# Optimization experiments

Measured on AMD Instinct MI355X. Metric: run time of the kernel, lower is better.

The kernel has to match this reference:

```python
import jax, jax.numpy as jnp
import numpy as np

H, N, F = 10, 200000, 128
HID, C = 256, 100
NEG_SLOPE = 0.2

def _leaky(x):
    return jnp.where(x >= 0, x, NEG_SLOPE * x)

def _prelu(x, a):
    return jnp.where(x >= 0, x, a * x)

def setup_inputs() -> dict:
    key = jax.random.key(0)
    ks = jax.random.split(key, 12)
    inp = {
        "features": jax.random.normal(ks[0], (H, N, F), dtype=jnp.float32),
        "label_emb": jax.random.normal(ks[1], (N, C), dtype=jnp.float32),
        # lr_att: Linear(2F, 1) -> weight as [2F] vector + scalar bias
        "W_att": jax.random.normal(ks[2], (2 * F,), dtype=jnp.float32) * 0.05,
        "b_att": jnp.zeros((), dtype=jnp.float32),
        # lr_output = FeedForwardNetII(F, HID, C, n_layers=2): Dense(F,HID), PReLU, Dense(HID,C)
        "Wo1": jax.random.normal(ks[3], (F, HID), dtype=jnp.float32) * 0.05,
        "bo1": jnp.zeros((HID,), dtype=jnp.float32),
        "ao": jnp.asarray(0.25, dtype=jnp.float32),
        "Wo2": jax.random.normal(ks[4], (HID, C), dtype=jnp.float32) * 0.05,
        "bo2": jnp.zeros((C,), dtype=jnp.float32),
        # label_fc = FeedForwardNet(C, HID, C, n_layers=2): Linear(C,HID), PReLU, Linear(HID,C)
        "Wl1": jax.random.normal(ks[5], (C, HID), dtype=jnp.float32) * 0.05,
        "bl1": jnp.zeros((HID,), dtype=jnp.float32),
        "al": jnp.asarray(0.25, dtype=jnp.float32),
        "Wl2": jax.random.normal(ks[6], (HID, C), dtype=jnp.float32) * 0.05,
        "bl2": jnp.zeros((C,), dtype=jnp.float32),
    }
    return inp

def reference(features, label_emb, W_att, b_att, Wo1, bo1, ao, Wo2, bo2,
              Wl1, bl1, al, Wl2, bl2):
    # features: [H, N, F]; dropouts are identity (p=0, eval mode)
    nF = features.shape[-1]
    W1, W2 = W_att[:nF], W_att[nF:]  # cat([history, x_i]) @ W_att == history@W1 + x_i@W2
    x0 = features[0]
    scores = [_leaky(x0 @ (W1 + W2) + b_att)]  # hop 0: cat([x0, x0])
    for i in range(1, features.shape[0]):
        hist_att = jax.nn.softmax(jnp.stack(scores, axis=1), axis=1)  # [N, i]
        history = jnp.einsum('ni,inf->nf', hist_att, features[:i])    # [N, F]
        scores.append(_leaky(history @ W1 + features[i] @ W2 + b_att))
    att = jax.nn.softmax(jnp.stack(scores, axis=1), axis=1)           # [N, H]
    right = jnp.einsum('ni,inf->nf', att, features)                   # [N, F]
    # lr_output: Dense -> PReLU -> Dense
    out = _prelu(right @ Wo1 + bo1, ao) @ Wo2 + bo2                   # [N, C]
    # label branch: label_fc(label_emb)
    out = out + (_prelu(label_emb @ Wl1 + bl1, al) @ Wl2 + bl2)
    return out
```

## Files before the change

kernel.cpp:

```cpp
#include <hip/hip_runtime.h>
#include <hip/hip_bf16.h>
#include <cstddef>

#define NHOP 10
#define NN 200000
#define FF 128
#define HIDD 256
#define CCC 100
#define NEG_SLOPE_C 0.2f

typedef __attribute__((ext_vector_type(8))) short bf16x8;
typedef __attribute__((ext_vector_type(4))) short bf16x4;
typedef __attribute__((ext_vector_type(4))) float f32x4;

__device__ __forceinline__ short f2bfs(float x){
  return __builtin_bit_cast(short, __float2bfloat16(x));
}
__device__ __forceinline__ float bf2f(short s){
  return __uint_as_float(((unsigned)(unsigned short)s) << 16);
}
__device__ __forceinline__ f32x4 mfma16(bf16x8 a, bf16x8 b, f32x4 c){
  return __builtin_amdgcn_mfma_f32_16x16x32_bf16(a, b, c, 0, 0, 0);
}
__device__ __forceinline__ float leakyf(float x){ return x >= 0.f ? x : NEG_SLOPE_C*x; }

__global__ __launch_bounds__(256) void prep_weights(
    const float* __restrict__ Wo1, const float* __restrict__ Wl1,
    const float* __restrict__ Wo2, const float* __restrict__ Wl2,
    unsigned short* __restrict__ Wo1T, unsigned short* __restrict__ Wl1T,
    unsigned short* __restrict__ Wo2T, unsigned short* __restrict__ Wl2T)
{
  const int id = blockIdx.x*256 + threadIdx.x;
  {
    const int c = id >> 7, k = id & 127;
    Wo1T[id] = (unsigned short)f2bfs(Wo1[(size_t)k*HIDD + c]);
    Wl1T[id] = (k < CCC) ? (unsigned short)f2bfs(Wl1[(size_t)k*HIDD + c]) : 0;
  }
  if (id < 112*256){
    const int c = id >> 8, k = id & 255;
    Wo2T[id] = (c < CCC) ? (unsigned short)f2bfs(Wo2[(size_t)k*CCC + c]) : 0;
    Wl2T[id] = (c < CCC) ? (unsigned short)f2bfs(Wl2[(size_t)k*CCC + c]) : 0;
  }
}

__global__ __launch_bounds__(256) void attn_right_kernel(
    const float* __restrict__ feat,
    const float* __restrict__ Watt,
    const float* __restrict__ batt,
    unsigned short* __restrict__ rightb)
{
  const int lane = threadIdx.x & 63;
  const int w = threadIdx.x >> 6;
  const int nl = lane >> 4, fl = lane & 15;
  const int n = blockIdx.x*16 + w*4 + nl;

  const float4 w1a = *reinterpret_cast<const float4*>(Watt + fl*4);
  const float4 w1b = *reinterpret_cast<const float4*>(Watt + 64 + fl*4);
  const float4 w2a = *reinterpret_cast<const float4*>(Watt + FF + fl*4);
  const float4 w2b = *reinterpret_cast<const float4*>(Watt + FF + 64 + fl*4);
  const float b = batt[0];

  float p1[NHOP], p2[NHOP];
  bf16x8 fbf[NHOP];
  const float* fp = feat + (size_t)n*FF;
  #pragma unroll
  for (int i=0;i<NHOP;i++){
    const float* hp = fp + (size_t)i*((size_t)NN*FF);
    const float4 va = *reinterpret_cast<const float4*>(hp + fl*4);
    const float4 vb = *reinterpret_cast<const float4*>(hp + 64 + fl*4);
    p1[i] = va.x*w1a.x + va.y*w1a.y + va.z*w1a.z + va.w*w1a.w
          + vb.x*w1b.x + vb.y*w1b.y + vb.z*w1b.z + vb.w*w1b.w;
    p2[i] = va.x*w2a.x + va.y*w2a.y + va.z*w2a.z + va.w*w2a.w
          + vb.x*w2b.x + vb.y*w2b.y + vb.z*w2b.z + vb.w*w2b.w;
    fbf[i][0]=f2bfs(va.x); fbf[i][1]=f2bfs(va.y); fbf[i][2]=f2bfs(va.z); fbf[i][3]=f2bfs(va.w);
    fbf[i][4]=f2bfs(vb.x); fbf[i][5]=f2bfs(vb.y); fbf[i][6]=f2bfs(vb.z); fbf[i][7]=f2bfs(vb.w);
  }
  #pragma unroll
  for (int m=8;m>0;m>>=1){
    #pragma unroll
    for (int i=0;i<NHOP;i++){
      p1[i] += __shfl_xor(p1[i], m, 64);
      p2[i] += __shfl_xor(p2[i], m, 64);
    }
  }
  float sc[NHOP];
  sc[0] = leakyf(p1[0] + p2[0] + b);
  #pragma unroll
  for (int i=1;i<NHOP;i++){
    float mx = sc[0];
    #pragma unroll
    for (int j=1;j<i;j++) mx = fmaxf(mx, sc[j]);
    float Z = 0.f, hs = 0.f;
    #pragma unroll
    for (int j=0;j<i;j++){
      const float e = __expf(sc[j]-mx);
      Z += e;
      hs = fmaf(e, p1[j], hs);
    }
    sc[i] = leakyf(hs/Z + p2[i] + b);
  }
  float mx = sc[0];
  #pragma unroll
  for (int j=1;j<NHOP;j++) mx = fmaxf(mx, sc[j]);
  float Z = 0.f;
  float e[NHOP];
  #pragma unroll
  for (int j=0;j<NHOP;j++){ e[j] = __expf(sc[j]-mx); Z += e[j]; }
  const float inv = 1.f/Z;
  float racc[8];
  #pragma unroll
  for (int u=0;u<8;u++) racc[u] = 0.f;
  #pragma unroll
  for (int j=0;j<NHOP;j++){
    const float a = e[j]*inv;
    #pragma unroll
    for (int u=0;u<8;u++) racc[u] = fmaf(a, bf2f(fbf[j][u]), racc[u]);
  }
  bf16x4 sa, sb;
  sa[0]=f2bfs(racc[0]); sa[1]=f2bfs(racc[1]); sa[2]=f2bfs(racc[2]); sa[3]=f2bfs(racc[3]);
  sb[0]=f2bfs(racc[4]); sb[1]=f2bfs(racc[5]); sb[2]=f2bfs(racc[6]); sb[3]=f2bfs(racc[7]);
  *reinterpret_cast<bf16x4*>(rightb + (size_t)n*FF + fl*4) = sa;
  *reinterpret_cast<bf16x4*>(rightb + (size_t)n*FF + 64 + fl*4) = sb;
}

__device__ __forceinline__ void mlp_branch(
    const unsigned short* sA, unsigned short* sH,
    const unsigned short* __restrict__ W1T, const float* __restrict__ b1, const float alpha,
    const unsigned short* __restrict__ W2T,
    f32x4 (&o)[2][4], const int w, const int lr, const int lq)
{
  bf16x8 B[4][4];
  float b1c[4];
  #pragma unroll
  for (int ctl=0; ctl<4; ++ctl){
    const int c = (4*w+ctl)*16 + lr;
    b1c[ctl] = b1[c];
    #pragma unroll
    for (int kk=0; kk<4; ++kk)
      B[ctl][kk] = *reinterpret_cast<const bf16x8*>(W1T + (size_t)c*128 + kk*32 + lq*8);
  }
  #pragma unroll
  for (int nt=0; nt<4; ++nt){
    f32x4 h[4];
    #pragma unroll
    for (int ctl=0; ctl<4; ++ctl) h[ctl] = (f32x4){0.f,0.f,0.f,0.f};
    const int row = nt*16 + lr;
    #pragma unroll
    for (int kk=0; kk<4; ++kk){
      const bf16x8 a = *reinterpret_cast<const bf16x8*>(
          (const char*)sA + row*256 + ((kk*64 + lq*16) ^ ((row&7)<<4)));
      #pragma unroll
      for (int ctl=0; ctl<4; ++ctl)
        h[ctl] = mfma16(a, B[ctl][kk], h[ctl]);
    }
    #pragma unroll
    for (int ctl=0; ctl<4; ++ctl){
      const int c = (4*w+ctl)*16 + lr;
      #pragma unroll
      for (int j=0; j<4; ++j){
        float v = h[ctl][j] + b1c[ctl];
        v = v >= 0.f ? v : alpha*v;
        const int n = nt*16 + lq*4 + j;
        *reinterpret_cast<unsigned short*>(
            (char*)sH + n*512 + ((2*c) ^ ((n&7)<<4))) = (unsigned short)f2bfs(v);
      }
    }
  }
  __syncthreads();
  #pragma unroll
  for (int i2=0; i2<2; ++i2){
    const int ct2 = 2*w + i2;
    if (ct2 < 7){
      bf16x8 b2[8];
      #pragma unroll
      for (int kk=0; kk<8; ++kk)
        b2[kk] = *reinterpret_cast<const bf16x8*>(W2T + (size_t)(ct2*16+lr)*256 + kk*32 + lq*8);
      #pragma unroll
      for (int nt=0; nt<4; ++nt){
        const int row = nt*16 + lr;
        #pragma unroll
        for (int kk=0; kk<8; ++kk){
          const bf16x8 a2 = *reinterpret_cast<const bf16x8*>(
              (const char*)sH + row*512 + ((kk*64 + lq*16) ^ ((row&7)<<4)));
          o[i2][nt] = mfma16(a2, b2[kk], o[i2][nt]);
        }
      }
    }
  }
}

__global__ __launch_bounds__(256) void mlp_mfma_kernel(
    const unsigned short* __restrict__ rightb, const float* __restrict__ label,
    const unsigned short* __restrict__ Wo1T, const float* __restrict__ bo1, const float* __restrict__ aop,
    const unsigned short* __restrict__ Wo2T, const float* __restrict__ bo2,
    const unsigned short* __restrict__ Wl1T, const float* __restrict__ bl1, const float* __restrict__ alp,
    const unsigned short* __restrict__ Wl2T, const float* __restrict__ bl2,
    float* __restrict__ out)
{
  __shared__ __align__(16) unsigned short sA[64*128];
  __shared__ __align__(16) unsigned short sH[64*256];
  const int t = threadIdx.x;
  const int w = t >> 6, lane = t & 63, lr = lane & 15, lq = lane >> 4;
  const size_t nb = (size_t)blockIdx.x * 64;

  f32x4 o[2][4];
  #pragma unroll
  for (int i2=0; i2<2; ++i2){
    const int ct2 = 2*w + i2;
    const int c2 = ct2*16 + lr;
    const float init = (ct2 < 7 && c2 < CCC) ? (bo2[c2] + bl2[c2]) : 0.f;
    #pragma unroll
    for (int nt=0; nt<4; ++nt) o[i2][nt] = (f32x4){init, init, init, init};
  }

  {
    const unsigned short* src = rightb + nb*FF;
    #pragma unroll
    for (int i=0;i<4;i++){
      const int chunk = t + 256*i;
      const int row = chunk >> 4, cs = chunk & 15;
      const bf16x8 v = *reinterpret_cast<const bf16x8*>(src + row*FF + cs*8);
      *reinterpret_cast<bf16x8*>((char*)sA + row*256 + ((cs*16) ^ ((row&7)<<4))) = v;
    }
  }
  __syncthreads();
  mlp_branch(sA, sH, Wo1T, bo1, aop[0], Wo2T, o, w, lr, lq);

  {
    #pragma unroll
    for (int i=0;i<7;i++){
      const int idx = t + 256*i;
      if (idx < 1600){
        const int row = idx/25, c0 = (idx%25)*4;
        const float4 v = *reinterpret_cast<const float4*>(label + (nb+row)*CCC + c0);
        bf16x4 p;
        p[0] = f2bfs(v.x); p[1] = f2bfs(v.y);
        p[2] = f2bfs(v.z); p[3] = f2bfs(v.w);
        *reinterpret_cast<bf16x4*>((char*)sA + row*256 + ((2*c0) ^ ((row&7)<<4))) = p;
      }
    }
    for (int idx = t; idx < 448; idx += 256){
      const int row = idx/7, ch = idx%7;
      *reinterpret_cast<bf16x4*>((char*)sA + row*256 + ((200 + 8*ch) ^ ((row&7)<<4))) = (bf16x4){0,0,0,0};
    }
  }
  __syncthreads();
  mlp_branch(sA, sH, Wl1T, bl1, alp[0], Wl2T, o, w, lr, lq);

  #pragma unroll
  for (int i2=0; i2<2; ++i2){
    const int ct2 = 2*w + i2;
    const int c2 = ct2*16 + lr;
    if (ct2 < 7 && c2 < CCC){
      #pragma unroll
      for (int nt=0; nt<4; ++nt){
        #pragma unroll
        for (int j=0; j<4; ++j){
          const int n = nt*16 + lq*4 + j;
          out[(nb + n)*CCC + c2] = o[i2][nt][j];
        }
      }
    }
  }
}

extern "C" void kernel_launch(void* const* d_in, const int* in_sizes, int n_in,
                              void* d_out, int out_size, void* d_ws, size_t ws_size,
                              hipStream_t stream) {
  const float* feat  = (const float*)d_in[0];
  const float* label = (const float*)d_in[1];
  const float* Watt  = (const float*)d_in[2];
  const float* batt  = (const float*)d_in[3];
  const float* Wo1   = (const float*)d_in[4];
  const float* bo1   = (const float*)d_in[5];
  const float* aop   = (const float*)d_in[6];
  const float* Wo2   = (const float*)d_in[7];
  const float* bo2   = (const float*)d_in[8];
  const float* Wl1   = (const float*)d_in[9];
  const float* bl1   = (const float*)d_in[10];
  const float* alp   = (const float*)d_in[11];
  const float* Wl2   = (const float*)d_in[12];
  const float* bl2   = (const float*)d_in[13];
  float* out = (float*)d_out;

  unsigned short* rightb = (unsigned short*)d_ws;
  unsigned short* Wo1T = rightb + (size_t)NN*FF;
  unsigned short* Wl1T = Wo1T + 256*128;
  unsigned short* Wo2T = Wl1T + 256*128;
  unsigned short* Wl2T = Wo2T + 112*256;

  prep_weights<<<128, 256, 0, stream>>>(Wo1, Wl1, Wo2, Wl2, Wo1T, Wl1T, Wo2T, Wl2T);
  attn_right_kernel<<<NN/16, 256, 0, stream>>>(feat, Watt, batt, rightb);
  mlp_mfma_kernel<<<NN/64, 256, 0, stream>>>(rightb, label,
                                             Wo1T, bo1, aop, Wo2T, bo2,
                                             Wl1T, bl1, alp, Wl2T, bl2, out);
}
```

Baseline: 346.6 us.

## Split second MLP GEMM across waves by node rows instead of output columns

```diff
diff --git a/kernel.cpp b/kernel.cpp
--- a/kernel.cpp
+++ b/kernel.cpp
@@ -123,11 +123,10 @@
   *reinterpret_cast<bf16x4*>(rightb + (size_t)n*FF + 64 + fl*4) = sb;
 }
 
-__device__ __forceinline__ void mlp_branch(
+__device__ __forceinline__ void gemm1_colsplit(
     const unsigned short* sA, unsigned short* sH,
     const unsigned short* __restrict__ W1T, const float* __restrict__ b1, const float alpha,
-    const unsigned short* __restrict__ W2T,
-    f32x4 (&o)[2][4], const int w, const int lr, const int lq)
+    const int w, const int lr, const int lq)
 {
   bf16x8 B[4][4];
   float b1c[4];
@@ -166,26 +165,27 @@
       }
     }
   }
-  __syncthreads();
-  #pragma unroll
-  for (int i2=0; i2<2; ++i2){
-    const int ct2 = 2*w + i2;
-    if (ct2 < 7){
-      bf16x8 b2[8];
-      #pragma unroll
-      for (int kk=0; kk<8; ++kk)
-        b2[kk] = *reinterpret_cast<const bf16x8*>(W2T + (size_t)(ct2*16+lr)*256 + kk*32 + lq*8);
-      #pragma unroll
-      for (int nt=0; nt<4; ++nt){
-        const int row = nt*16 + lr;
-        #pragma unroll
-        for (int kk=0; kk<8; ++kk){
-          const bf16x8 a2 = *reinterpret_cast<const bf16x8*>(
-              (const char*)sH + row*512 + ((kk*64 + lq*16) ^ ((row&7)<<4)));
-          o[i2][nt] = mfma16(a2, b2[kk], o[i2][nt]);
-        }
-      }
-    }
+}
+
+__device__ __forceinline__ void gemm2_nodesplit(const unsigned short* sH,
+    const unsigned short* __restrict__ W2T, f32x4 (&o)[7],
+    const int w, const int lr, const int lq)
+{
+  const int row = w*16 + lr;
+  bf16x8 a2[8];
+  #pragma unroll
+  for (int kk=0; kk<8; ++kk)
+    a2[kk] = *reinterpret_cast<const bf16x8*>(
+        (const char*)sH + row*512 + ((kk*64 + lq*16) ^ ((row&7)<<4)));
+  #pragma unroll
+  for (int ct=0; ct<7; ++ct){
+    bf16x8 b2[8];
+    #pragma unroll
+    for (int kk=0; kk<8; ++kk)
+      b2[kk] = *reinterpret_cast<const bf16x8*>(W2T + (size_t)(ct*16+lr)*256 + kk*32 + lq*8);
+    #pragma unroll
+    for (int kk=0; kk<8; ++kk)
+      o[ct] = mfma16(a2[kk], b2[kk], o[ct]);
   }
 }
 
@@ -203,14 +203,12 @@
   const int w = t >> 6, lane = t & 63, lr = lane & 15, lq = lane >> 4;
   const size_t nb = (size_t)blockIdx.x * 64;
 
-  f32x4 o[2][4];
-  #pragma unroll
-  for (int i2=0; i2<2; ++i2){
-    const int ct2 = 2*w + i2;
-    const int c2 = ct2*16 + lr;
-    const float init = (ct2 < 7 && c2 < CCC) ? (bo2[c2] + bl2[c2]) : 0.f;
-    #pragma unroll
-    for (int nt=0; nt<4; ++nt) o[i2][nt] = (f32x4){init, init, init, init};
+  f32x4 o[7];
+  #pragma unroll
+  for (int ct=0; ct<7; ++ct){
+    const int c2 = ct*16 + lr;
+    const float init = (c2 < CCC) ? (bo2[c2] + bl2[c2]) : 0.f;
+    o[ct] = (f32x4){init, init, init, init};
   }
 
   {
@@ -224,7 +222,9 @@
     }
   }
   __syncthreads();
-  mlp_branch(sA, sH, Wo1T, bo1, aop[0], Wo2T, o, w, lr, lq);
+
+  gemm1_colsplit(sA, sH, Wo1T, bo1, aop[0], w, lr, lq);
+  __syncthreads();
 
   {
     #pragma unroll
@@ -244,21 +244,21 @@
       *reinterpret_cast<bf16x4*>((char*)sA + row*256 + ((200 + 8*ch) ^ ((row&7)<<4))) = (bf16x4){0,0,0,0};
     }
   }
-  __syncthreads();
-  mlp_branch(sA, sH, Wl1T, bl1, alp[0], Wl2T, o, w, lr, lq);
-
-  #pragma unroll
-  for (int i2=0; i2<2; ++i2){
-    const int ct2 = 2*w + i2;
-    const int c2 = ct2*16 + lr;
-    if (ct2 < 7 && c2 < CCC){
+  gemm2_nodesplit(sH, Wo2T, o, w, lr, lq);
+  __syncthreads();
+
+  gemm1_colsplit(sA, sH, Wl1T, bl1, alp[0], w, lr, lq);
+  __syncthreads();
+  gemm2_nodesplit(sH, Wl2T, o, w, lr, lq);
+
+  #pragma unroll
+  for (int ct=0; ct<7; ++ct){
+    const int c2 = ct*16 + lr;
+    if (c2 < CCC){
       #pragma unroll
-      for (int nt=0; nt<4; ++nt){
-        #pragma unroll
-        for (int j=0; j<4; ++j){
-          const int n = nt*16 + lq*4 + j;
-          out[(nb + n)*CCC + c2] = o[i2][nt][j];
-        }
+      for (int j=0; j<4; ++j){
+        const int n = w*16 + lq*4 + j;
+        out[(nb + n)*CCC + c2] = o[ct][j];
       }
     }
   }
```

Result: slower. 446.1 us (+28.7%).

## Fuse attention and MLP into one kernel with 16-row tiles

Applied to the files above, without the earlier changes.

```diff
diff --git a/kernel.cpp b/kernel.cpp
--- a/kernel.cpp
+++ b/kernel.cpp
@@ -43,91 +43,10 @@
   }
 }
 
-__global__ __launch_bounds__(256) void attn_right_kernel(
-    const float* __restrict__ feat,
-    const float* __restrict__ Watt,
-    const float* __restrict__ batt,
-    unsigned short* __restrict__ rightb)
-{
-  const int lane = threadIdx.x & 63;
-  const int w = threadIdx.x >> 6;
-  const int nl = lane >> 4, fl = lane & 15;
-  const int n = blockIdx.x*16 + w*4 + nl;
-
-  const float4 w1a = *reinterpret_cast<const float4*>(Watt + fl*4);
-  const float4 w1b = *reinterpret_cast<const float4*>(Watt + 64 + fl*4);
-  const float4 w2a = *reinterpret_cast<const float4*>(Watt + FF + fl*4);
-  const float4 w2b = *reinterpret_cast<const float4*>(Watt + FF + 64 + fl*4);
-  const float b = batt[0];
-
-  float p1[NHOP], p2[NHOP];
-  bf16x8 fbf[NHOP];
-  const float* fp = feat + (size_t)n*FF;
-  #pragma unroll
-  for (int i=0;i<NHOP;i++){
-    const float* hp = fp + (size_t)i*((size_t)NN*FF);
-    const float4 va = *reinterpret_cast<const float4*>(hp + fl*4);
-    const float4 vb = *reinterpret_cast<const float4*>(hp + 64 + fl*4);
-    p1[i] = va.x*w1a.x + va.y*w1a.y + va.z*w1a.z + va.w*w1a.w
-          + vb.x*w1b.x + vb.y*w1b.y + vb.z*w1b.z + vb.w*w1b.w;
-    p2[i] = va.x*w2a.x + va.y*w2a.y + va.z*w2a.z + va.w*w2a.w
-          + vb.x*w2b.x + vb.y*w2b.y + vb.z*w2b.z + vb.w*w2b.w;
-    fbf[i][0]=f2bfs(va.x); fbf[i][1]=f2bfs(va.y); fbf[i][2]=f2bfs(va.z); fbf[i][3]=f2bfs(va.w);
-    fbf[i][4]=f2bfs(vb.x); fbf[i][5]=f2bfs(vb.y); fbf[i][6]=f2bfs(vb.z); fbf[i][7]=f2bfs(vb.w);
-  }
-  #pragma unroll
-  for (int m=8;m>0;m>>=1){
-    #pragma unroll
-    for (int i=0;i<NHOP;i++){
-      p1[i] += __shfl_xor(p1[i], m, 64);
-      p2[i] += __shfl_xor(p2[i], m, 64);
-    }
-  }
-  float sc[NHOP];
-  sc[0] = leakyf(p1[0] + p2[0] + b);
-  #pragma unroll
-  for (int i=1;i<NHOP;i++){
-    float mx = sc[0];
-    #pragma unroll
-    for (int j=1;j<i;j++) mx = fmaxf(mx, sc[j]);
-    float Z = 0.f, hs = 0.f;
-    #pragma unroll
-    for (int j=0;j<i;j++){
-      const float e = __expf(sc[j]-mx);
-      Z += e;
-      hs = fmaf(e, p1[j], hs);
-    }
-    sc[i] = leakyf(hs/Z + p2[i] + b);
-  }
-  float mx = sc[0];
-  #pragma unroll
-  for (int j=1;j<NHOP;j++) mx = fmaxf(mx, sc[j]);
-  float Z = 0.f;
-  float e[NHOP];
-  #pragma unroll
-  for (int j=0;j<NHOP;j++){ e[j] = __expf(sc[j]-mx); Z += e[j]; }
-  const float inv = 1.f/Z;
-  float racc[8];
-  #pragma unroll
-  for (int u=0;u<8;u++) racc[u] = 0.f;
-  #pragma unroll
-  for (int j=0;j<NHOP;j++){
-    const float a = e[j]*inv;
-    #pragma unroll
-    for (int u=0;u<8;u++) racc[u] = fmaf(a, bf2f(fbf[j][u]), racc[u]);
-  }
-  bf16x4 sa, sb;
-  sa[0]=f2bfs(racc[0]); sa[1]=f2bfs(racc[1]); sa[2]=f2bfs(racc[2]); sa[3]=f2bfs(racc[3]);
-  sb[0]=f2bfs(racc[4]); sb[1]=f2bfs(racc[5]); sb[2]=f2bfs(racc[6]); sb[3]=f2bfs(racc[7]);
-  *reinterpret_cast<bf16x4*>(rightb + (size_t)n*FF + fl*4) = sa;
-  *reinterpret_cast<bf16x4*>(rightb + (size_t)n*FF + 64 + fl*4) = sb;
-}
-
-__device__ __forceinline__ void mlp_branch(
+__device__ __forceinline__ void g1_16(
     const unsigned short* sA, unsigned short* sH,
     const unsigned short* __restrict__ W1T, const float* __restrict__ b1, const float alpha,
-    const unsigned short* __restrict__ W2T,
-    f32x4 (&o)[2][4], const int w, const int lr, const int lq)
+    const int w, const int lr, const int lq)
 {
   bf16x8 B[4][4];
   float b1c[4];
@@ -139,126 +58,186 @@
     for (int kk=0; kk<4; ++kk)
       B[ctl][kk] = *reinterpret_cast<const bf16x8*>(W1T + (size_t)c*128 + kk*32 + lq*8);
   }
-  #pragma unroll
-  for (int nt=0; nt<4; ++nt){
-    f32x4 h[4];
-    #pragma unroll
-    for (int ctl=0; ctl<4; ++ctl) h[ctl] = (f32x4){0.f,0.f,0.f,0.f};
-    const int row = nt*16 + lr;
-    #pragma unroll
-    for (int kk=0; kk<4; ++kk){
-      const bf16x8 a = *reinterpret_cast<const bf16x8*>(
-          (const char*)sA + row*256 + ((kk*64 + lq*16) ^ ((row&7)<<4)));
-      #pragma unroll
-      for (int ctl=0; ctl<4; ++ctl)
-        h[ctl] = mfma16(a, B[ctl][kk], h[ctl]);
-    }
-    #pragma unroll
-    for (int ctl=0; ctl<4; ++ctl){
-      const int c = (4*w+ctl)*16 + lr;
-      #pragma unroll
-      for (int j=0; j<4; ++j){
-        float v = h[ctl][j] + b1c[ctl];
-        v = v >= 0.f ? v : alpha*v;
-        const int n = nt*16 + lq*4 + j;
-        *reinterpret_cast<unsigned short*>(
-            (char*)sH + n*512 + ((2*c) ^ ((n&7)<<4))) = (unsigned short)f2bfs(v);
-      }
-    }
-  }
-  __syncthreads();
+  f32x4 h[4];
+  #pragma unroll
+  for (int ctl=0; ctl<4; ++ctl) h[ctl] = (f32x4){0.f,0.f,0.f,0.f};
+  #pragma unroll
+  for (int kk=0; kk<4; ++kk){
+    const bf16x8 a = *reinterpret_cast<const bf16x8*>(
+        (const char*)sA + lr*256 + ((kk*64 + lq*16) ^ ((lr&7)<<4)));
+    #pragma unroll
+    for (int ctl=0; ctl<4; ++ctl)
+      h[ctl] = mfma16(a, B[ctl][kk], h[ctl]);
+  }
+  #pragma unroll
+  for (int ctl=0; ctl<4; ++ctl){
+    const int c = (4*w+ctl)*16 + lr;
+    #pragma unroll
+    for (int j=0; j<4; ++j){
+      float v = h[ctl][j] + b1c[ctl];
+      v = v >= 0.f ? v : alpha*v;
+      const int n = lq*4 + j;
+      *reinterpret_cast<unsigned short*>(
+          (char*)sH + n*512 + ((2*c) ^ ((n&7)<<4))) = (unsigned short)f2bfs(v);
+    }
+  }
+}
+
+__device__ __forceinline__ void g2_16(const unsigned short* sH,
+    const unsigned short* __restrict__ W2T, f32x4 (&o)[2],
+    const int w, const int lr, const int lq)
+{
+  bf16x8 a2[8];
+  #pragma unroll
+  for (int kk=0; kk<8; ++kk)
+    a2[kk] = *reinterpret_cast<const bf16x8*>(
+        (const char*)sH + lr*512 + ((kk*64 + lq*16) ^ ((lr&7)<<4)));
   #pragma unroll
   for (int i2=0; i2<2; ++i2){
-    const int ct2 = 2*w + i2;
+    const int ct2 = w + 4*i2;
     if (ct2 < 7){
-      bf16x8 b2[8];
-      #pragma unroll
-      for (int kk=0; kk<8; ++kk)
-        b2[kk] = *reinterpret_cast<const bf16x8*>(W2T + (size_t)(ct2*16+lr)*256 + kk*32 + lq*8);
-      #pragma unroll
-      for (int nt=0; nt<4; ++nt){
-        const int row = nt*16 + lr;
-        #pragma unroll
-        for (int kk=0; kk<8; ++kk){
-          const bf16x8 a2 = *reinterpret_cast<const bf16x8*>(
-              (const char*)sH + row*512 + ((kk*64 + lq*16) ^ ((row&7)<<4)));
-          o[i2][nt] = mfma16(a2, b2[kk], o[i2][nt]);
-        }
-      }
-    }
-  }
-}
-
-__global__ __launch_bounds__(256) void mlp_mfma_kernel(
-    const unsigned short* __restrict__ rightb, const float* __restrict__ label,
+      #pragma unroll
+      for (int kk=0; kk<8; ++kk){
+        const bf16x8 b2 = *reinterpret_cast<const bf16x8*>(
+            W2T + (size_t)(ct2*16+lr)*256 + kk*32 + lq*8);
+        o[i2] = mfma16(a2[kk], b2, o[i2]);
+      }
+    }
+  }
+}
+
+__global__ __launch_bounds__(256) void gamlp_fused16(
+    const float* __restrict__ feat, const float* __restrict__ label,
+    const float* __restrict__ Watt, const float* __restrict__ batt,
     const unsigned short* __restrict__ Wo1T, const float* __restrict__ bo1, const float* __restrict__ aop,
     const unsigned short* __restrict__ Wo2T, const float* __restrict__ bo2,
     const unsigned short* __restrict__ Wl1T, const float* __restrict__ bl1, const float* __restrict__ alp,
     const unsigned short* __restrict__ Wl2T, const float* __restrict__ bl2,
     float* __restrict__ out)
 {
-  __shared__ __align__(16) unsigned short sA[64*128];
-  __shared__ __align__(16) unsigned short sH[64*256];
+  __shared__ __align__(16) unsigned short sA[16*128];
+  __shared__ __align__(16) unsigned short sH[16*256];
   const int t = threadIdx.x;
-  const int w = t >> 6, lane = t & 63, lr = lane & 15, lq = lane >> 4;
-  const size_t nb = (size_t)blockIdx.x * 64;
-
-  f32x4 o[2][4];
+  const int w = t >> 6, lane = t & 63;
+  const int nl = lane >> 4, fl = lane & 15;
+  const int lr = lane & 15, lq = lane >> 4;
+  const size_t nb = (size_t)blockIdx.x * 16;
+
+  {
+    const int n = (int)nb + w*4 + nl;
+    const float4 w1a = *reinterpret_cast<const float4*>(Watt + fl*4);
+    const float4 w1b = *reinterpret_cast<const float4*>(Watt + 64 + fl*4);
+    const float4 w2a = *reinterpret_cast<const float4*>(Watt + FF + fl*4);
+    const float4 w2b = *reinterpret_cast<const float4*>(Watt + FF + 64 + fl*4);
+    const float b = batt[0];
+
+    float p1[NHOP], p2[NHOP];
+    bf16x8 fbf[NHOP];
+    const float* fp = feat + (size_t)n*FF;
+    #pragma unroll
+    for (int i=0;i<NHOP;i++){
+      const float* hp = fp + (size_t)i*((size_t)NN*FF);
+      const float4 va = *reinterpret_cast<const float4*>(hp + fl*4);
+      const float4 vb = *reinterpret_cast<const float4*>(hp + 64 + fl*4);
+      p1[i] = va.x*w1a.x + va.y*w1a.y + va.z*w1a.z + va.w*w1a.w
+            + vb.x*w1b.x + vb.y*w1b.y + vb.z*w1b.z + vb.w*w1b.w;
+      p2[i] = va.x*w2a.x + va.y*w2a.y + va.z*w2a.z + va.w*w2a.w
+            + vb.x*w2b.x + vb.y*w2b.y + vb.z*w2b.z + vb.w*w2b.w;
+      fbf[i][0]=f2bfs(va.x); fbf[i][1]=f2bfs(va.y); fbf[i][2]=f2bfs(va.z); fbf[i][3]=f2bfs(va.w);
+      fbf[i][4]=f2bfs(vb.x); fbf[i][5]=f2bfs(vb.y); fbf[i][6]=f2bfs(vb.z); fbf[i][7]=f2bfs(vb.w);
+    }
+    #pragma unroll
+    for (int m=8;m>0;m>>=1){
+      #pragma unroll
+      for (int i=0;i<NHOP;i++){
+        p1[i] += __shfl_xor(p1[i], m, 64);
+        p2[i] += __shfl_xor(p2[i], m, 64);
+      }
+    }
+    float sc[NHOP];
+    sc[0] = leakyf(p1[0] + p2[0] + b);
+    #pragma unroll
+    for (int i=1;i<NHOP;i++){
+      float mx = sc[0];
+      #pragma unroll
+      for (int j=1;j<i;j++) mx = fmaxf(mx, sc[j]);
+      float Z = 0.f, hs = 0.f;
+      #pragma unroll
+      for (int j=0;j<i;j++){
+        const float e = __expf(sc[j]-mx);
+        Z += e;
+        hs = fmaf(e, p1[j], hs);
+      }
+      sc[i] = leakyf(hs/Z + p2[i] + b);
+    }
+    float mx = sc[0];
+    #pragma unroll
+    for (int j=1;j<NHOP;j++) mx = fmaxf(mx, sc[j]);
+    float Z = 0.f;
+    float e[NHOP];
+    #pragma unroll
+    for (int j=0;j<NHOP;j++){ e[j] = __expf(sc[j]-mx); Z += e[j]; }
+    const float inv = 1.f/Z;
+    float racc[8];
+    #pragma unroll
+    for (int u=0;u<8;u++) racc[u] = 0.f;
+    #pragma unroll
+    for (int j=0;j<NHOP;j++){
+      const float a = e[j]*inv;
+      #pragma unroll
+      for (int u=0;u<8;u++) racc[u] = fmaf(a, bf2f(fbf[j][u]), racc[u]);
+    }
+    bf16x4 sa, sb;
+    sa[0]=f2bfs(racc[0]); sa[1]=f2bfs(racc[1]); sa[2]=f2bfs(racc[2]); sa[3]=f2bfs(racc[3]);
+    sb[0]=f2bfs(racc[4]); sb[1]=f2bfs(racc[5]); sb[2]=f2bfs(racc[6]); sb[3]=f2bfs(racc[7]);
+    const int row = w*4 + nl;
+    *reinterpret_cast<bf16x4*>((char*)sA + row*256 + ((fl*8) ^ ((row&7)<<4))) = sa;
+    *reinterpret_cast<bf16x4*>((char*)sA + row*256 + ((128 + fl*8) ^ ((row&7)<<4))) = sb;
+  }
+  __syncthreads();
+
+  f32x4 o[2];
   #pragma unroll
   for (int i2=0; i2<2; ++i2){
-    const int ct2 = 2*w + i2;
+    const int ct2 = w + 4*i2;
     const int c2 = ct2*16 + lr;
     const float init = (ct2 < 7 && c2 < CCC) ? (bo2[c2] + bl2[c2]) : 0.f;
-    #pragma unroll
-    for (int nt=0; nt<4; ++nt) o[i2][nt] = (f32x4){init, init, init, init};
-  }
+    o[i2] = (f32x4){init, init, init, init};
+  }
+
+  g1_16(sA, sH, Wo1T, bo1, aop[0], w, lr, lq);
+  __syncthreads();
 
   {
-    const unsigned short* src = rightb + nb*FF;
-    #pragma unroll
-    for (int i=0;i<4;i++){
-      const int chunk = t + 256*i;
-      const int row = chunk >> 4, cs = chunk & 15;
-      const bf16x8 v = *reinterpret_cast<const bf16x8*>(src + row*FF + cs*8);
-      *reinterpret_cast<bf16x8*>((char*)sA + row*256 + ((cs*16) ^ ((row&7)<<4))) = v;
-    }
-  }
-  __syncthreads();
-  mlp_branch(sA, sH, Wo1T, bo1, aop[0], Wo2T, o, w, lr, lq);
-
-  {
-    #pragma unroll
-    for (int i=0;i<7;i++){
-      const int idx = t + 256*i;
-      if (idx < 1600){
-        const int row = idx/25, c0 = (idx%25)*4;
-        const float4 v = *reinterpret_cast<const float4*>(label + (nb+row)*CCC + c0);
-        bf16x4 p;
-        p[0] = f2bfs(v.x); p[1] = f2bfs(v.y);
-        p[2] = f2bfs(v.z); p[3] = f2bfs(v.w);
-        *reinterpret_cast<bf16x4*>((char*)sA + row*256 + ((2*c0) ^ ((row&7)<<4))) = p;
-      }
-    }
-    for (int idx = t; idx < 448; idx += 256){
-      const int row = idx/7, ch = idx%7;
+    for (int idx = t; idx < 400; idx += 256){
+      const int row = idx/25, c0 = (idx%25)*4;
+      const float4 v = *reinterpret_cast<const float4*>(label + (nb+row)*CCC + c0);
+      bf16x4 p;
+      p[0] = f2bfs(v.x); p[1] = f2bfs(v.y);
+      p[2] = f2bfs(v.z); p[3] = f2bfs(v.w);
+      *reinterpret_cast<bf16x4*>((char*)sA + row*256 + ((2*c0) ^ ((row&7)<<4))) = p;
+    }
+    if (t < 112){
+      const int row = t/7, ch = t%7;
       *reinterpret_cast<bf16x4*>((char*)sA + row*256 + ((200 + 8*ch) ^ ((row&7)<<4))) = (bf16x4){0,0,0,0};
     }
   }
-  __syncthreads();
-  mlp_branch(sA, sH, Wl1T, bl1, alp[0], Wl2T, o, w, lr, lq);
+  g2_16(sH, Wo2T, o, w, lr, lq);
+  __syncthreads();
+
+  g1_16(sA, sH, Wl1T, bl1, alp[0], w, lr, lq);
+  __syncthreads();
+  g2_16(sH, Wl2T, o, w, lr, lq);
 
   #pragma unroll
   for (int i2=0; i2<2; ++i2){
-    const int ct2 = 2*w + i2;
+    const int ct2 = w + 4*i2;
     const int c2 = ct2*16 + lr;
     if (ct2 < 7 && c2 < CCC){
       #pragma unroll
-      for (int nt=0; nt<4; ++nt){
-        #pragma unroll
-        for (int j=0; j<4; ++j){
-          const int n = nt*16 + lq*4 + j;
-          out[(nb + n)*CCC + c2] = o[i2][nt][j];
-        }
+      for (int j=0; j<4; ++j){
+        const int n = lq*4 + j;
+        out[(nb + n)*CCC + c2] = o[i2][j];
       }
     }
   }
@@ -283,15 +262,13 @@
   const float* bl2   = (const float*)d_in[13];
   float* out = (float*)d_out;
 
-  unsigned short* rightb = (unsigned short*)d_ws;
-  unsigned short* Wo1T = rightb + (size_t)NN*FF;
+  unsigned short* Wo1T = (unsigned short*)d_ws;
   unsigned short* Wl1T = Wo1T + 256*128;
   unsigned short* Wo2T = Wl1T + 256*128;
   unsigned short* Wl2T = Wo2T + 112*256;
 
   prep_weights<<<128, 256, 0, stream>>>(Wo1, Wl1, Wo2, Wl2, Wo1T, Wl1T, Wo2T, Wl2T);
-  attn_right_kernel<<<NN/16, 256, 0, stream>>>(feat, Watt, batt, rightb);
-  mlp_mfma_kernel<<<NN/64, 256, 0, stream>>>(rightb, label,
-                                             Wo1T, bo1, aop, Wo2T, bo2,
-                                             Wl1T, bl1, alp, Wl2T, bl2, out);
-}
+  gamlp_fused16<<<NN/16, 256, 0, stream>>>(feat, label, Watt, batt,
+                                           Wo1T, bo1, aop, Wo2T, bo2,
+                                           Wl1T, bl1, alp, Wl2T, bl2, out);
+}
```

Result: slower. 544.2 us (+57.0%).

## Shrink MLP kernel tile to 32 rows and overlap label staging with second GEMM

Applied to the files above, without the earlier changes.

```diff
diff --git a/kernel.cpp b/kernel.cpp
--- a/kernel.cpp
+++ b/kernel.cpp
@@ -123,73 +123,80 @@
   *reinterpret_cast<bf16x4*>(rightb + (size_t)n*FF + 64 + fl*4) = sb;
 }
 
-__device__ __forceinline__ void mlp_branch(
+__device__ __forceinline__ void g1_32(
     const unsigned short* sA, unsigned short* sH,
     const unsigned short* __restrict__ W1T, const float* __restrict__ b1, const float alpha,
-    const unsigned short* __restrict__ W2T,
-    f32x4 (&o)[2][4], const int w, const int lr, const int lq)
-{
-  bf16x8 B[4][4];
-  float b1c[4];
-  #pragma unroll
-  for (int ctl=0; ctl<4; ++ctl){
-    const int c = (4*w+ctl)*16 + lr;
-    b1c[ctl] = b1[c];
-    #pragma unroll
-    for (int kk=0; kk<4; ++kk)
-      B[ctl][kk] = *reinterpret_cast<const bf16x8*>(W1T + (size_t)c*128 + kk*32 + lq*8);
-  }
-  #pragma unroll
-  for (int nt=0; nt<4; ++nt){
-    f32x4 h[4];
-    #pragma unroll
-    for (int ctl=0; ctl<4; ++ctl) h[ctl] = (f32x4){0.f,0.f,0.f,0.f};
+    const int w, const int lr, const int lq)
+{
+  #pragma unroll
+  for (int cc=0; cc<2; ++cc){
+    bf16x8 B[2][4];
+    float b1c[2];
+    #pragma unroll
+    for (int ct=0; ct<2; ++ct){
+      const int c = (4*w + cc*2 + ct)*16 + lr;
+      b1c[ct] = b1[c];
+      #pragma unroll
+      for (int kk=0; kk<4; ++kk)
+        B[ct][kk] = *reinterpret_cast<const bf16x8*>(W1T + (size_t)c*128 + kk*32 + lq*8);
+    }
+    #pragma unroll
+    for (int nt=0; nt<2; ++nt){
+      const int row = nt*16 + lr;
+      f32x4 h0 = (f32x4){0.f,0.f,0.f,0.f}, h1 = h0;
+      #pragma unroll
+      for (int kk=0; kk<4; ++kk){
+        const bf16x8 a = *reinterpret_cast<const bf16x8*>(
+            (const char*)sA + row*256 + ((kk*64 + lq*16) ^ ((row&7)<<4)));
+        h0 = mfma16(a, B[0][kk], h0);
+        h1 = mfma16(a, B[1][kk], h1);
+      }
+      #pragma unroll
+      for (int ct=0; ct<2; ++ct){
+        const int c = (4*w + cc*2 + ct)*16 + lr;
+        const f32x4 hv = ct ? h1 : h0;
+        #pragma unroll
+        for (int j=0; j<4; ++j){
+          float v = hv[j] + b1c[ct];
+          v = v >= 0.f ? v : alpha*v;
+          const int nrow = nt*16 + lq*4 + j;
+          *reinterpret_cast<unsigned short*>(
+              (char*)sH + nrow*512 + ((2*c) ^ ((nrow&7)<<4))) = (unsigned short)f2bfs(v);
+        }
+      }
+    }
+  }
+}
+
+__device__ __forceinline__ void g2_32(const unsigned short* sH,
+    const unsigned short* __restrict__ W2T, f32x4 (&o)[2][2],
+    const int w, const int lr, const int lq)
+{
+  bf16x8 a2[2][8];
+  #pragma unroll
+  for (int nt=0; nt<2; ++nt){
     const int row = nt*16 + lr;
     #pragma unroll
-    for (int kk=0; kk<4; ++kk){
-      const bf16x8 a = *reinterpret_cast<const bf16x8*>(
-          (const char*)sA + row*256 + ((kk*64 + lq*16) ^ ((row&7)<<4)));
-      #pragma unroll
-      for (int ctl=0; ctl<4; ++ctl)
-        h[ctl] = mfma16(a, B[ctl][kk], h[ctl]);
-    }
-    #pragma unroll
-    for (int ctl=0; ctl<4; ++ctl){
-      const int c = (4*w+ctl)*16 + lr;
-      #pragma unroll
-      for (int j=0; j<4; ++j){
-        float v = h[ctl][j] + b1c[ctl];
-        v = v >= 0.f ? v : alpha*v;
-        const int n = nt*16 + lq*4 + j;
-        *reinterpret_cast<unsigned short*>(
-            (char*)sH + n*512 + ((2*c) ^ ((n&7)<<4))) = (unsigned short)f2bfs(v);
-      }
-    }
-  }
-  __syncthreads();
+    for (int kk=0; kk<8; ++kk)
+      a2[nt][kk] = *reinterpret_cast<const bf16x8*>(
+          (const char*)sH + row*512 + ((kk*64 + lq*16) ^ ((row&7)<<4)));
+  }
   #pragma unroll
   for (int i2=0; i2<2; ++i2){
     const int ct2 = 2*w + i2;
     if (ct2 < 7){
-      bf16x8 b2[8];
-      #pragma unroll
-      for (int kk=0; kk<8; ++kk)
-        b2[kk] = *reinterpret_cast<const bf16x8*>(W2T + (size_t)(ct2*16+lr)*256 + kk*32 + lq*8);
-      #pragma unroll
-      for (int nt=0; nt<4; ++nt){
-        const int row = nt*16 + lr;
-        #pragma unroll
-        for (int kk=0; kk<8; ++kk){
-          const bf16x8 a2 = *reinterpret_cast<const bf16x8*>(
-              (const char*)sH + row*512 + ((kk*64 + lq*16) ^ ((row&7)<<4)));
-          o[i2][nt] = mfma16(a2, b2[kk], o[i2][nt]);
-        }
+      #pragma unroll
+      for (int kk=0; kk<8; ++kk){
+        const bf16x8 b2 = *reinterpret_cast<const bf16x8*>(
+            W2T + (size_t)(ct2*16+lr)*256 + kk*32 + lq*8);
+        o[i2][0] = mfma16(a2[0][kk], b2, o[i2][0]);
+        o[i2][1] = mfma16(a2[1][kk], b2, o[i2][1]);
       }
     }
   }
 }
 
-__global__ __launch_bounds__(256) void mlp_mfma_kernel(
+__global__ __launch_bounds__(256) void mlp_mfma32_kernel(
     const unsigned short* __restrict__ rightb, const float* __restrict__ label,
     const unsigned short* __restrict__ Wo1T, const float* __restrict__ bo1, const float* __restrict__ aop,
     const unsigned short* __restrict__ Wo2T, const float* __restrict__ bo2,
@@ -197,26 +204,27 @@
     const unsigned short* __restrict__ Wl2T, const float* __restrict__ bl2,
     float* __restrict__ out)
 {
-  __shared__ __align__(16) unsigned short sA[64*128];
-  __shared__ __align__(16) unsigned short sH[64*256];
+  __shared__ __align__(16) unsigned short sA[32*128];
+  __shared__ __align__(16) unsigned short sH[32*256];
   const int t = threadIdx.x;
   const int w = t >> 6, lane = t & 63, lr = lane & 15, lq = lane >> 4;
-  const size_t nb = (size_t)blockIdx.x * 64;
-
-  f32x4 o[2][4];
+  const size_t nb = (size_t)blockIdx.x * 32;
+  const float ao = aop[0], al = alp[0];
+
+  f32x4 o[2][2];
   #pragma unroll
   for (int i2=0; i2<2; ++i2){
     const int ct2 = 2*w + i2;
     const int c2 = ct2*16 + lr;
     const float init = (ct2 < 7 && c2 < CCC) ? (bo2[c2] + bl2[c2]) : 0.f;
-    #pragma unroll
-    for (int nt=0; nt<4; ++nt) o[i2][nt] = (f32x4){init, init, init, init};
+    o[i2][0] = (f32x4){init, init, init, init};
+    o[i2][1] = o[i2][0];
   }
 
   {
     const unsigned short* src = rightb + nb*FF;
     #pragma unroll
-    for (int i=0;i<4;i++){
+    for (int i=0;i<2;i++){
       const int chunk = t + 256*i;
       const int row = chunk >> 4, cs = chunk & 15;
       const bf16x8 v = *reinterpret_cast<const bf16x8*>(src + row*FF + cs*8);
@@ -224,28 +232,30 @@
     }
   }
   __syncthreads();
-  mlp_branch(sA, sH, Wo1T, bo1, aop[0], Wo2T, o, w, lr, lq);
+
+  g1_32(sA, sH, Wo1T, bo1, ao, w, lr, lq);
+  __syncthreads();
 
   {
-    #pragma unroll
-    for (int i=0;i<7;i++){
-      const int idx = t + 256*i;
-      if (idx < 1600){
-        const int row = idx/25, c0 = (idx%25)*4;
-        const float4 v = *reinterpret_cast<const float4*>(label + (nb+row)*CCC + c0);
-        bf16x4 p;
-        p[0] = f2bfs(v.x); p[1] = f2bfs(v.y);
-        p[2] = f2bfs(v.z); p[3] = f2bfs(v.w);
-        *reinterpret_cast<bf16x4*>((char*)sA + row*256 + ((2*c0) ^ ((row&7)<<4))) = p;
-      }
-    }
-    for (int idx = t; idx < 448; idx += 256){
-      const int row = idx/7, ch = idx%7;
+    for (int idx = t; idx < 800; idx += 256){
+      const int row = idx/25, c0 = (idx%25)*4;
+      const float4 v = *reinterpret_cast<const float4*>(label + (nb+row)*CCC + c0);
+      bf16x4 p;
+      p[0] = f2bfs(v.x); p[1] = f2bfs(v.y);
+      p[2] = f2bfs(v.z); p[3] = f2bfs(v.w);
+      *reinterpret_cast<bf16x4*>((char*)sA + row*256 + ((2*c0) ^ ((row&7)<<4))) = p;
+    }
+    if (t < 224){
+      const int row = t/7, ch = t%7;
       *reinterpret_cast<bf16x4*>((char*)sA + row*256 + ((200 + 8*ch) ^ ((row&7)<<4))) = (bf16x4){0,0,0,0};
     }
   }
+  g2_32(sH, Wo2T, o, w, lr, lq);
   __syncthreads();
-  mlp_branch(sA, sH, Wl1T, bl1, alp[0], Wl2T, o, w, lr, lq);
+
+  g1_32(sA, sH, Wl1T, bl1, al, w, lr, lq);
+  __syncthreads();
+  g2_32(sH, Wl2T, o, w, lr, lq);
 
   #pragma unroll
   for (int i2=0; i2<2; ++i2){
@@ -253,7 +263,7 @@
     const int c2 = ct2*16 + lr;
     if (ct2 < 7 && c2 < CCC){
       #pragma unroll
-      for (int nt=0; nt<4; ++nt){
+      for (int nt=0; nt<2; ++nt){
         #pragma unroll
         for (int j=0; j<4; ++j){
           const int n = nt*16 + lq*4 + j;
@@ -291,7 +301,7 @@
 
   prep_weights<<<128, 256, 0, stream>>>(Wo1, Wl1, Wo2, Wl2, Wo1T, Wl1T, Wo2T, Wl2T);
   attn_right_kernel<<<NN/16, 256, 0, stream>>>(feat, Watt, batt, rightb);
-  mlp_mfma_kernel<<<NN/64, 256, 0, stream>>>(rightb, label,
-                                             Wo1T, bo1, aop, Wo2T, bo2,
-                                             Wl1T, bl1, alp, Wl2T, bl2, out);
-}
+  mlp_mfma32_kernel<<<NN/32, 256, 0, stream>>>(rightb, label,
+                                               Wo1T, bo1, aop, Wo2T, bo2,
+                                               Wl1T, bl1, alp, Wl2T, bl2, out);
+}
```

New measurement: 425.0 us. +22.6%, slower.
